# Performance work log

Hardware: AMD Instinct MI355X
Metric: run time of the kernel (lower is better)

The kernel has to match this reference:

```python
import jax, jax.numpy as jnp
import numpy as np

B, C, T, H, HI = 256, 64, 512, 8, 3


def setup_inputs() -> dict:
    key = jax.random.key(0)
    ks = jax.random.split(key, 20)
    s = 0.1
    return {
        "x": jax.random.normal(ks[0], (B, C, T), jnp.float32),
        "m": jax.random.uniform(ks[1], (B, C, T), jnp.float32),
        "d": jax.random.uniform(ks[2], (B, C, T), jnp.float32),
        # interpolater params (per-channel blocks of the block-diagonal matrices)
        "Wf": jax.random.normal(ks[3], (C, H, H), jnp.float32) * s,
        "Vf": jax.random.normal(ks[4], (C, H, 3), jnp.float32) * s,
        "cf": jax.random.normal(ks[5], (C, H), jnp.float32) * s,
        "Wb": jax.random.normal(ks[6], (C, H, H), jnp.float32) * s,
        "Vb": jax.random.normal(ks[7], (C, H, 3), jnp.float32) * s,
        "cb": jax.random.normal(ks[8], (C, H), jnp.float32) * s,
        "U": jax.random.normal(ks[9], (C, 2 * H), jnp.float32) * s,
        "c0": jax.random.normal(ks[10], (C,), jnp.float32) * s,
        # imputer params (nn.Linear: y = x @ W.T + b)
        "V1_w": jax.random.normal(ks[11], (HI, C), jnp.float32) * s,
        "V2_w": jax.random.normal(ks[12], (HI, C), jnp.float32) * s,
        "U_w": jax.random.normal(ks[13], (HI, C), jnp.float32) * s,
        "U_b": jax.random.normal(ks[14], (HI,), jnp.float32) * s,
        "W_w": jax.random.normal(ks[15], (C, HI), jnp.float32) * s,
        "W_b": jax.random.normal(ks[16], (C,), jnp.float32) * s,
    }


def _mrnn_forward(x, m, d, Wf, Vf, cf, Wb, Vb, cb, U, c0,
                  V1_w, V2_w, U_w, U_b, W_w, W_b):
    act = jax.nn.relu
    Bv, Cv, Tv = x.shape
    Hv = Wf.shape[-1]
    # replication pad along time: [B,C,T] -> [B,C,T+2]
    pad = lambda a: jnp.pad(a, ((0, 0), (0, 0), (1, 1)), mode='edge')
    s = jnp.stack([pad(x), pad(m), pad(d)], axis=-1)        # [B,C,T+2,3]
    # forward scan consumes padded times 0..T-1; backward consumes T+1 down to 2
    in_f = jnp.moveaxis(s[:, :, :Tv], 2, 0)                 # [T,B,C,3]
    in_b = jnp.moveaxis(s[:, :, 2:Tv + 2][:, :, ::-1], 2, 0)  # [T,B,C,3]

    def make_step(W, V, c):
        def step(h, inp):  # h:[B,C,H] inp:[B,C,3]
            hn = act(jnp.einsum('chk,bck->bch', W, h)
                     + jnp.einsum('chj,bcj->bch', V, inp) + c)
            return hn, hn
        return step

    h0 = jnp.zeros((Bv, Cv, Hv), x.dtype)
    _, hf = jax.lax.scan(make_step(Wf, Vf, cf), h0, in_f)   # [T,B,C,H]
    _, hb = jax.lax.scan(make_step(Wb, Vb, cb), h0, in_b)
    hb = hb[::-1]  # align backward hiddens with time index

    x_est = act(jnp.einsum('ch,tbch->bct', U[:, :Hv], hf)
                + jnp.einsum('ch,tbch->bct', U[:, Hv:], hb)
                + c0[None, :, None])                        # [B,C,T]

    # imputer (time as batch dim); U weight has zeroed diagonal
    idx = jnp.arange(min(U_w.shape[0], Cv))
    Uz = U_w.at[idx, idx].set(0.0)
    h = act(jnp.swapaxes(x_est, 1, 2) @ V1_w.T
            + jnp.swapaxes(m, 1, 2) @ V2_w.T
            + jnp.swapaxes(x, 1, 2) @ Uz.T + U_b)           # [B,T,HI]
    out = h @ W_w.T + W_b                                   # [B,T,C]
    return jnp.swapaxes(out, 1, 2)                          # [B,C,T]


def reference(x, m, d, Wf, Vf, cf, Wb, Vb, cb, U, c0,
              V1_w, V2_w, U_w, U_b, W_w, W_b):
    return _mrnn_forward(x, m, d, Wf, Vf, cf, Wb, Vb, cb, U, c0,
                         V1_w, V2_w, U_w, U_b, W_w, W_b)
```

## Files before the change

kernel.cpp:

```cpp
#include <hip/hip_runtime.h>

constexpr int Tn = 512;
constexpr int Cn = 64;
constexpr int NS = 16384;

__device__ __forceinline__ float dpp_swap1(float v) {
    int i = __builtin_bit_cast(int, v);
    i = __builtin_amdgcn_mov_dpp(i, 0xB1 , 0xF, 0xF, true);
    return __builtin_bit_cast(float, i);
}

#define GRP_F(X4, M4, P4) do {                                        \
    op[0*NS] = step(cx, cm, cd);                                      \
    op[1*NS] = step((X4).x, (M4).x, (P4).x);                          \
    op[2*NS] = step((X4).y, (M4).y, (P4).y);                          \
    op[3*NS] = step((X4).z, (M4).z, (P4).z);                          \
    op += 4*NS;                                                       \
    cx = (X4).w; cm = (M4).w; cd = (P4).w;                            \
} while (0)

#define GRP_B(X4, M4, P4) do {                                        \
    op[0]      = step(cx, cm, cd);                                    \
    op[-1*NS]  = step((X4).w, (M4).w, (P4).w);                        \
    op[-2*NS]  = step((X4).z, (M4).z, (P4).z);                        \
    op[-3*NS]  = step((X4).y, (M4).y, (P4).y);                        \
    op -= 4*NS;                                                       \
    cx = (X4).x; cm = (M4).x; cd = (P4).x;                            \
} while (0)

__global__ __launch_bounds__(256, 1) void mrnn_scan(
    const float* __restrict__ x, const float* __restrict__ m, const float* __restrict__ d,
    const float* __restrict__ Wf, const float* __restrict__ Vf, const float* __restrict__ cf,
    const float* __restrict__ Wb, const float* __restrict__ Vb, const float* __restrict__ cbk,
    const float* __restrict__ Uu, float* __restrict__ accF, float* __restrict__ accB)
{
    const int g   = blockIdx.x * blockDim.x + threadIdx.x;
    const int ph  = g & 1;
    const int ch  = g >> 1;
    const int c   = ch & 63;
    const int b   = (ch >> 6) & 255;
    const int dir = ch >> 14;

    const float* W  = dir ? Wb  : Wf;
    const float* V  = dir ? Vb  : Vf;
    const float* cc = dir ? cbk : cf;

    const int ob = 4 * ph;
    const int pb = 4 - ob;
    float Wo[4][4], Wpr[4][4], Vx[4], Vm[4], Vd[4], cb4[4], Uv[4];
    #pragma unroll
    for (int j = 0; j < 4; ++j) {
        const int r = ob + j;
        const float* Wr = W + c*64 + r*8;
        #pragma unroll
        for (int k = 0; k < 4; ++k) {
            Wo[j][k]  = Wr[ob + k];
            Wpr[j][k] = Wr[pb + k];
        }
        Vx[j]  = V[c*24 + r*3 + 0];
        Vm[j]  = V[c*24 + r*3 + 1];
        Vd[j]  = V[c*24 + r*3 + 2];
        cb4[j] = cc[c*8 + r];
        Uv[j]  = Uu[c*16 + dir*8 + r];
    }

    float h0 = 0.f, h1 = 0.f, h2 = 0.f, h3 = 0.f;
    float cx, cm, cd;
    const size_t base = ((size_t)b * Cn + c) * Tn;
    const float4* x4p = (const float4*)(x + base);
    const float4* m4p = (const float4*)(m + base);
    const float4* d4p = (const float4*)(d + base);
    float* op = (dir ? accB : accF) + b*64 + c;

    auto step = [&](float xv, float mv, float dv) -> float {
        const float p0 = dpp_swap1(h0);
        const float p1 = dpp_swap1(h1);
        const float p2 = dpp_swap1(h2);
        const float p3 = dpp_swap1(h3);
        float n[4];
        #pragma unroll
        for (int j = 0; j < 4; ++j) {
            float sA = fmaf(Vx[j], xv, cb4[j]);
            float sB = Vm[j] * mv;
            float sC = Vd[j] * dv;
            sA = fmaf(Wo[j][0], h0, sA);
            sB = fmaf(Wo[j][1], h1, sB);
            sC = fmaf(Wo[j][2], h2, sC);
            sA = fmaf(Wo[j][3], h3, sA);
            sB = fmaf(Wpr[j][0], p0, sB);
            sC = fmaf(Wpr[j][1], p1, sC);
            sA = fmaf(Wpr[j][2], p2, sA);
            sB = fmaf(Wpr[j][3], p3, sB);
            n[j] = fmaxf(sA + (sB + sC), 0.f);
        }
        h0 = n[0]; h1 = n[1]; h2 = n[2]; h3 = n[3];
        float dot = fmaf(Uv[0], h0, Uv[1] * h1) + fmaf(Uv[2], h2, Uv[3] * h3);
        dot += dpp_swap1(dot);
        return dot;
    };

    if (dir == 0) {
        float4 X0 = x4p[0], X1 = x4p[1], X2 = x4p[2], X3 = x4p[3];
        float4 M0 = m4p[0], M1 = m4p[1], M2 = m4p[2], M3 = m4p[3];
        float4 P0 = d4p[0], P1 = d4p[1], P2 = d4p[2], P3 = d4p[3];
        cx = X0.x; cm = M0.x; cd = P0.x;
        #pragma unroll 1
        for (int i = 0; i < 31; ++i) {
            float4 tX, tM, tP;
            tX = x4p[4*i+4]; tM = m4p[4*i+4]; tP = d4p[4*i+4];
            GRP_F(X0, M0, P0);  X0 = tX; M0 = tM; P0 = tP;
            tX = x4p[4*i+5]; tM = m4p[4*i+5]; tP = d4p[4*i+5];
            GRP_F(X1, M1, P1);  X1 = tX; M1 = tM; P1 = tP;
            tX = x4p[4*i+6]; tM = m4p[4*i+6]; tP = d4p[4*i+6];
            GRP_F(X2, M2, P2);  X2 = tX; M2 = tM; P2 = tP;
            tX = x4p[4*i+7]; tM = m4p[4*i+7]; tP = d4p[4*i+7];
            GRP_F(X3, M3, P3);  X3 = tX; M3 = tM; P3 = tP;
        }
        GRP_F(X0, M0, P0); GRP_F(X1, M1, P1);
        GRP_F(X2, M2, P2); GRP_F(X3, M3, P3);
    } else {
        op += 511 * NS;
        float4 X0 = x4p[127], X1 = x4p[126], X2 = x4p[125], X3 = x4p[124];
        float4 M0 = m4p[127], M1 = m4p[126], M2 = m4p[125], M3 = m4p[124];
        float4 P0 = d4p[127], P1 = d4p[126], P2 = d4p[125], P3 = d4p[124];
        cx = X0.w; cm = M0.w; cd = P0.w;
        #pragma unroll 1
        for (int i = 0; i < 31; ++i) {
            float4 tX, tM, tP;
            tX = x4p[123-4*i]; tM = m4p[123-4*i]; tP = d4p[123-4*i];
            GRP_B(X0, M0, P0);  X0 = tX; M0 = tM; P0 = tP;
            tX = x4p[122-4*i]; tM = m4p[122-4*i]; tP = d4p[122-4*i];
            GRP_B(X1, M1, P1);  X1 = tX; M1 = tM; P1 = tP;
            tX = x4p[121-4*i]; tM = m4p[121-4*i]; tP = d4p[121-4*i];
            GRP_B(X2, M2, P2);  X2 = tX; M2 = tM; P2 = tP;
            tX = x4p[120-4*i]; tM = m4p[120-4*i]; tP = d4p[120-4*i];
            GRP_B(X3, M3, P3);  X3 = tX; M3 = tM; P3 = tP;
        }
        GRP_B(X0, M0, P0); GRP_B(X1, M1, P1);
        GRP_B(X2, M2, P2); GRP_B(X3, M3, P3);
    }
}

__global__ __launch_bounds__(256, 2) void mrnn_mix(
    const float* __restrict__ x, const float* __restrict__ m,
    const float* __restrict__ accF, const float* __restrict__ accB,
    const float* __restrict__ c0, const float* __restrict__ V1w,
    const float* __restrict__ V2w, const float* __restrict__ Uw,
    const float* __restrict__ Ub, const float* __restrict__ Ww,
    const float* __restrict__ Wbias, float* __restrict__ out)
{
    const int bt = blockIdx.x * 256 + threadIdx.x;
    const int b = bt >> 9;
    const int t = bt & 511;

    const float4* aF4 = (const float4*)(accF + (size_t)t * NS + b * Cn);
    const float4* aB4 = (const float4*)(accB + (size_t)t * NS + b * Cn);
    const size_t xb = (size_t)b * (Cn * Tn) + t;

    float h0 = Ub[0], h1 = Ub[1], h2 = Ub[2];
    #pragma unroll
    for (int c4 = 0; c4 < 16; ++c4) {
        const float4 fa = aF4[c4];
        const float4 fb = aB4[c4];
        const float fav[4] = {fa.x, fa.y, fa.z, fa.w};
        const float fbv[4] = {fb.x, fb.y, fb.z, fb.w};
        #pragma unroll
        for (int j = 0; j < 4; ++j) {
            const int cch = 4*c4 + j;
            const float xe = fmaxf(fav[j] + fbv[j] + c0[cch], 0.f);
            const float mv = m[xb + (size_t)cch * Tn];
            const float xv = x[xb + (size_t)cch * Tn];
            const float u0 = (cch == 0) ? 0.f : Uw[0*Cn + cch];
            const float u1 = (cch == 1) ? 0.f : Uw[1*Cn + cch];
            const float u2 = (cch == 2) ? 0.f : Uw[2*Cn + cch];
            h0 += V1w[0*Cn + cch]*xe + V2w[0*Cn + cch]*mv + u0*xv;
            h1 += V1w[1*Cn + cch]*xe + V2w[1*Cn + cch]*mv + u1*xv;
            h2 += V1w[2*Cn + cch]*xe + V2w[2*Cn + cch]*mv + u2*xv;
        }
    }
    h0 = fmaxf(h0, 0.f); h1 = fmaxf(h1, 0.f); h2 = fmaxf(h2, 0.f);

    float* opt = out + (size_t)b * (Cn * Tn) + t;
    #pragma unroll
    for (int cch = 0; cch < Cn; ++cch) {
        opt[(size_t)cch * Tn] = Wbias[cch] + Ww[cch*3 + 0]*h0 + Ww[cch*3 + 1]*h1 + Ww[cch*3 + 2]*h2;
    }
}

extern "C" void kernel_launch(void* const* d_in, const int* in_sizes, int n_in,
                              void* d_out, int out_size, void* d_ws, size_t ws_size,
                              hipStream_t stream)
{
    const float* x   = (const float*)d_in[0];
    const float* m   = (const float*)d_in[1];
    const float* d   = (const float*)d_in[2];
    const float* Wf  = (const float*)d_in[3];
    const float* Vf  = (const float*)d_in[4];
    const float* cf  = (const float*)d_in[5];
    const float* Wb  = (const float*)d_in[6];
    const float* Vb  = (const float*)d_in[7];
    const float* cb  = (const float*)d_in[8];
    const float* U   = (const float*)d_in[9];
    const float* c0  = (const float*)d_in[10];
    const float* V1w = (const float*)d_in[11];
    const float* V2w = (const float*)d_in[12];
    const float* Uw  = (const float*)d_in[13];
    const float* Ub  = (const float*)d_in[14];
    const float* Ww  = (const float*)d_in[15];
    const float* Wb_ = (const float*)d_in[16];
    float* out = (float*)d_out;

    float* accF = (float*)d_ws;
    float* accB = accF + (size_t)Tn * NS;

    mrnn_scan<<<256, 256, 0, stream>>>(x, m, d, Wf, Vf, cf, Wb, Vb, cb, U, accF, accB);
    mrnn_mix<<<512, 256, 0, stream>>>(x, m, accF, accB, c0, V1w, V2w, Uw, Ub, Ww, Wb_, out);
}
```

Baseline: 118.0 us.

## Split each RNN sequence over four lanes using packed fp16 dot2 math

Each sequence's 8-wide hidden state is now spread over 4 lanes, two rows per lane, instead of 2 lanes. The recurrence uses packed fp16 v_dot2 instructions with DPP rotations to gather neighbours' hidden values. Each lane now stores only one of every four timesteps' outputs, which spreads the stores across lanes. This doubles the thread count (512 blocks, launch bounds 2) and shortens the per-step dependency chain. The cost is fp16 rounding of weights and hidden state, which accumulates over the 512-step recurrence and may break accuracy tolerance. It also adds more DPP traffic per step.

After: 111.2 us. -5.7%, faster.

```diff
diff --git a/kernel.cpp b/kernel.cpp
--- a/kernel.cpp
+++ b/kernel.cpp
@@ -4,102 +4,130 @@
 constexpr int Cn = 64;
 constexpr int NS = 16384;
 
-__device__ __forceinline__ float dpp_swap1(float v) {
+typedef _Float16 h2 __attribute__((ext_vector_type(2)));
+
+__device__ __forceinline__ h2 pkrtz(float lo, float hi) {
+    return __builtin_bit_cast(h2, __builtin_amdgcn_cvt_pkrtz(lo, hi));
+}
+__device__ __forceinline__ float fdot2h(h2 a, h2 b, float c) {
+#if __has_builtin(__builtin_amdgcn_fdot2)
+    return __builtin_amdgcn_fdot2(a, b, c, false);
+#else
+    return (float)a.x * (float)b.x + (float)a.y * (float)b.y + c;
+#endif
+}
+template<int CTRL>
+__device__ __forceinline__ float dppf(float v) {
     int i = __builtin_bit_cast(int, v);
-    i = __builtin_amdgcn_mov_dpp(i, 0xB1 , 0xF, 0xF, true);
+    i = __builtin_amdgcn_mov_dpp(i, CTRL, 0xF, 0xF, true);
     return __builtin_bit_cast(float, i);
 }
+template<int CTRL>
+__device__ __forceinline__ h2 dpph(h2 v) {
+    int i = __builtin_bit_cast(int, v);
+    i = __builtin_amdgcn_mov_dpp(i, CTRL, 0xF, 0xF, true);
+    return __builtin_bit_cast(h2, i);
+}
 
 #define GRP_F(X4, M4, P4) do {                                        \
-    op[0*NS] = step(cx, cm, cd);                                      \
-    op[1*NS] = step((X4).x, (M4).x, (P4).x);                          \
-    op[2*NS] = step((X4).y, (M4).y, (P4).y);                          \
-    op[3*NS] = step((X4).z, (M4).z, (P4).z);                          \
-    op += 4*NS;                                                       \
+    float s0 = step(cx, cm, cd);                                      \
+    float s1 = step((X4).x, (M4).x, (P4).x);                          \
+    float s2 = step((X4).y, (M4).y, (P4).y);                          \
+    float s3 = step((X4).z, (M4).z, (P4).z);                          \
+    *opq = fmaf(a3, s3, fmaf(a2, s2, fmaf(a1, s1, a0 * s0)));         \
+    opq += 4 * NS;                                                    \
     cx = (X4).w; cm = (M4).w; cd = (P4).w;                            \
 } while (0)
 
 #define GRP_B(X4, M4, P4) do {                                        \
-    op[0]      = step(cx, cm, cd);                                    \
-    op[-1*NS]  = step((X4).w, (M4).w, (P4).w);                        \
-    op[-2*NS]  = step((X4).z, (M4).z, (P4).z);                        \
-    op[-3*NS]  = step((X4).y, (M4).y, (P4).y);                        \
-    op -= 4*NS;                                                       \
+    float s0 = step(cx, cm, cd);                                      \
+    float s1 = step((X4).w, (M4).w, (P4).w);                          \
+    float s2 = step((X4).z, (M4).z, (P4).z);                          \
+    float s3 = step((X4).y, (M4).y, (P4).y);                          \
+    *opq = fmaf(a3, s3, fmaf(a2, s2, fmaf(a1, s1, a0 * s0)));         \
+    opq -= 4 * NS;                                                    \
     cx = (X4).x; cm = (M4).x; cd = (P4).x;                            \
 } while (0)
 
-__global__ __launch_bounds__(256, 1) void mrnn_scan(
+__global__ __launch_bounds__(256, 2) void mrnn_scan(
     const float* __restrict__ x, const float* __restrict__ m, const float* __restrict__ d,
     const float* __restrict__ Wf, const float* __restrict__ Vf, const float* __restrict__ cf,
     const float* __restrict__ Wb, const float* __restrict__ Vb, const float* __restrict__ cbk,
     const float* __restrict__ Uu, float* __restrict__ accF, float* __restrict__ accB)
 {
-    const int g   = blockIdx.x * blockDim.x + threadIdx.x;
-    const int ph  = g & 1;
-    const int ch  = g >> 1;
-    const int c   = ch & 63;
-    const int b   = (ch >> 6) & 255;
-    const int dir = ch >> 14;
+    const int w    = blockIdx.x * 4 + (threadIdx.x >> 6);
+    const int lane = threadIdx.x & 63;
+    const int q    = lane & 3;
+    const int cl   = lane >> 2;
+    const int dir  = w >> 10;
+    const int rem  = w & 1023;
+    const int b    = rem >> 2;
+    const int c    = (rem & 3) * 16 + cl;
 
     const float* W  = dir ? Wb  : Wf;
     const float* V  = dir ? Vb  : Vf;
     const float* cc = dir ? cbk : cf;
 
-    const int ob = 4 * ph;
-    const int pb = 4 - ob;
-    float Wo[4][4], Wpr[4][4], Vx[4], Vm[4], Vd[4], cb4[4], Uv[4];
-    #pragma unroll
-    for (int j = 0; j < 4; ++j) {
-        const int r = ob + j;
-        const float* Wr = W + c*64 + r*8;
+    const int r0 = 2*q, r1 = 2*q + 1;
+
+    h2 W00, W01, W02, W03, W10, W11, W12, W13, VA0, VB0, VA1, VB1, UP;
+    {
+        const float* Wc = W + c*64;
         #pragma unroll
-        for (int k = 0; k < 4; ++k) {
-            Wo[j][k]  = Wr[ob + k];
-            Wpr[j][k] = Wr[pb + k];
-        }
-        Vx[j]  = V[c*24 + r*3 + 0];
-        Vm[j]  = V[c*24 + r*3 + 1];
-        Vd[j]  = V[c*24 + r*3 + 2];
-        cb4[j] = cc[c*8 + r];
-        Uv[j]  = Uu[c*16 + dir*8 + r];
-    }
-
-    float h0 = 0.f, h1 = 0.f, h2 = 0.f, h3 = 0.f;
+        for (int j = 0; j < 4; ++j) {
+            const int s2 = 2 * ((q + j) & 3);
+            h2 w0; w0.x = (_Float16)Wc[r0*8 + s2]; w0.y = (_Float16)Wc[r0*8 + s2 + 1];
+            h2 w1; w1.x = (_Float16)Wc[r1*8 + s2]; w1.y = (_Float16)Wc[r1*8 + s2 + 1];
+            if (j == 0) { W00 = w0; W10 = w1; }
+            else if (j == 1) { W01 = w0; W11 = w1; }
+            else if (j == 2) { W02 = w0; W12 = w1; }
+            else { W03 = w0; W13 = w1; }
+        }
+        VA0.x = (_Float16)V[c*24 + r0*3 + 0]; VA0.y = (_Float16)V[c*24 + r0*3 + 1];
+        VB0.x = (_Float16)V[c*24 + r0*3 + 2]; VB0.y = (_Float16)cc[c*8 + r0];
+        VA1.x = (_Float16)V[c*24 + r1*3 + 0]; VA1.y = (_Float16)V[c*24 + r1*3 + 1];
+        VB1.x = (_Float16)V[c*24 + r1*3 + 2]; VB1.y = (_Float16)cc[c*8 + r1];
+        UP.x  = (_Float16)Uu[c*16 + dir*8 + r0];
+        UP.y  = (_Float16)Uu[c*16 + dir*8 + r1];
+    }
+
+    const float a0 = (q == 0) ? 1.f : 0.f;
+    const float a1 = (q == 1) ? 1.f : 0.f;
+    const float a2 = (q == 2) ? 1.f : 0.f;
+    const float a3 = (q == 3) ? 1.f : 0.f;
+
+    h2 hp = {(_Float16)0.f, (_Float16)0.f};
     float cx, cm, cd;
     const size_t base = ((size_t)b * Cn + c) * Tn;
     const float4* x4p = (const float4*)(x + base);
     const float4* m4p = (const float4*)(m + base);
     const float4* d4p = (const float4*)(d + base);
-    float* op = (dir ? accB : accF) + b*64 + c;
+    const int seq = b * 64 + c;
 
     auto step = [&](float xv, float mv, float dv) -> float {
-        const float p0 = dpp_swap1(h0);
-        const float p1 = dpp_swap1(h1);
-        const float p2 = dpp_swap1(h2);
-        const float p3 = dpp_swap1(h3);
-        float n[4];
-        #pragma unroll
-        for (int j = 0; j < 4; ++j) {
-            float sA = fmaf(Vx[j], xv, cb4[j]);
-            float sB = Vm[j] * mv;
-            float sC = Vd[j] * dv;
-            sA = fmaf(Wo[j][0], h0, sA);
-            sB = fmaf(Wo[j][1], h1, sB);
-            sC = fmaf(Wo[j][2], h2, sC);
-            sA = fmaf(Wo[j][3], h3, sA);
-            sB = fmaf(Wpr[j][0], p0, sB);
-            sC = fmaf(Wpr[j][1], p1, sC);
-            sA = fmaf(Wpr[j][2], p2, sA);
-            sB = fmaf(Wpr[j][3], p3, sB);
-            n[j] = fmaxf(sA + (sB + sC), 0.f);
-        }
-        h0 = n[0]; h1 = n[1]; h2 = n[2]; h3 = n[3];
-        float dot = fmaf(Uv[0], h0, Uv[1] * h1) + fmaf(Uv[2], h2, Uv[3] * h3);
-        dot += dpp_swap1(dot);
-        return dot;
+        h2 iA = pkrtz(xv, mv);
+        h2 iB = pkrtz(dv, 1.0f);
+        h2 p0 = hp;
+        h2 p1 = dpph<0x39>(p0);
+        h2 p2 = dpph<0x39>(p1);
+        h2 p3 = dpph<0x39>(p2);
+        float r0v = fdot2h(VA0, iA, fdot2h(VB0, iB, 0.f));
+        float r1v = fdot2h(VA1, iA, fdot2h(VB1, iB, 0.f));
+        r0v = fdot2h(W00, p0, r0v);  r1v = fdot2h(W10, p0, r1v);
+        r0v = fdot2h(W01, p1, r0v);  r1v = fdot2h(W11, p1, r1v);
+        r0v = fdot2h(W02, p2, r0v);  r1v = fdot2h(W12, p2, r1v);
+        r0v = fdot2h(W03, p3, r0v);  r1v = fdot2h(W13, p3, r1v);
+        r0v = fmaxf(r0v, 0.f);
+        r1v = fmaxf(r1v, 0.f);
+        hp = pkrtz(r0v, r1v);
+        float du = fdot2h(UP, hp, 0.f);
+        du += dppf<0xB1>(du);
+        du += dppf<0x4E>(du);
+        return du;
     };
 
     if (dir == 0) {
+        float* opq = accF + seq + (size_t)q * NS;
         float4 X0 = x4p[0], X1 = x4p[1], X2 = x4p[2], X3 = x4p[3];
         float4 M0 = m4p[0], M1 = m4p[1], M2 = m4p[2], M3 = m4p[3];
         float4 P0 = d4p[0], P1 = d4p[1], P2 = d4p[2], P3 = d4p[3];
@@ -119,7 +147,7 @@
         GRP_F(X0, M0, P0); GRP_F(X1, M1, P1);
         GRP_F(X2, M2, P2); GRP_F(X3, M3, P3);
     } else {
-        op += 511 * NS;
+        float* opq = accB + seq + (size_t)(511 - q) * NS;
         float4 X0 = x4p[127], X1 = x4p[126], X2 = x4p[125], X3 = x4p[124];
         float4 M0 = m4p[127], M1 = m4p[126], M2 = m4p[125], M3 = m4p[124];
         float4 P0 = d4p[127], P1 = d4p[126], P2 = d4p[125], P3 = d4p[124];
@@ -213,6 +241,6 @@
     float* accF = (float*)d_ws;
     float* accB = accF + (size_t)Tn * NS;
 
-    mrnn_scan<<<256, 256, 0, stream>>>(x, m, d, Wf, Vf, cf, Wb, Vb, cb, U, accF, accB);
+    mrnn_scan<<<512, 256, 0, stream>>>(x, m, d, Wf, Vf, cf, Wb, Vb, cb, U, accF, accB);
     mrnn_mix<<<512, 256, 0, stream>>>(x, m, accF, accB, c0, V1w, V2w, Uw, Ub, Ww, Wb_, out);
 }
```
